# Performance work log

Hardware: AMD Instinct MI355X
Metric: run time of the kernel (lower is better)

The kernel has to match this reference:

```python
import jax, jax.numpy as jnp
import numpy as np

VOL = 128
FACTOR = 0.5 * VOL
N = 262144
LAT = 16
B = 8


def setup_inputs() -> dict:
    key = jax.random.key(0)
    ks = jax.random.split(key, 10)
    x = jax.random.normal(ks[0], (B, LAT), jnp.float32)
    inds = jax.random.randint(ks[1], (N, 3), 1, 126, dtype=jnp.int32)
    reference_values = jax.random.normal(ks[2], (N,), jnp.float32)
    # SIREN first layer: U(-1/in, 1/in)
    W0 = jax.random.uniform(ks[3], (LAT, 8), jnp.float32, -1.0 / LAT, 1.0 / LAT)
    b0 = jnp.zeros((8,), jnp.float32)
    # SIREN hidden layers (4 residual layers): U(-sqrt(6/in), sqrt(6/in))
    lim_h = float(np.sqrt(6.0 / 8.0))
    Wh = jax.random.uniform(ks[4], (4, 8, 8), jnp.float32, -lim_h, lim_h)
    bh = jnp.zeros((4, 8), jnp.float32)
    # final glorot-uniform layer: 8 -> 4N
    lim_f = float(np.sqrt(6.0 / (8.0 + 4.0 * N)))
    Wf = jax.random.uniform(ks[5], (8, 4 * N), jnp.float32, -lim_f, lim_f)
    bf = jnp.zeros((4 * N,), jnp.float32)
    return {"x": x, "W0": W0, "b0": b0, "Wh": Wh, "bh": bh, "Wf": Wf,
            "bf": bf, "reference_values": reference_values, "inds": inds}


def _siren_mlp(x, W0, b0, Wh, bh, Wf, bf):
    bf16 = jnp.bfloat16
    h = jnp.sin(30.0 * (x.astype(bf16) @ W0.astype(bf16) + b0.astype(bf16)))
    for i in range(Wh.shape[0]):  # 4 residual sine layers, 8-wide
        h = h + jnp.sin(h @ Wh[i].astype(bf16) + bh[i].astype(bf16))
    return h.astype(jnp.float32) @ Wf + bf  # [B, 4N], final layer in fp32


def reference(x, W0, b0, Wh, bh, Wf, bf, reference_values, inds):
    Bn = x.shape[0]
    out = _siren_mlp(x, W0, b0, Wh, bh, Wf, bf).reshape(Bn, N, 4)
    delta_coords, delta_values = out[..., :3], out[..., 3]
    # coords = stack(z,y,x reversed) normalized to [-1,1)
    coords_norm = (jnp.stack([inds[:, 2], inds[:, 1], inds[:, 0]], axis=1)
                   .astype(jnp.float32) - FACTOR) / FACTOR  # [N,3]
    values = reference_values + delta_values                 # [B,N]
    coords = FACTOR * (coords_norm[None] + delta_coords) + FACTOR  # [B,N,3]
    bposf = jnp.floor(coords)
    bposi = bposf.astype(jnp.int32)
    f = coords - bposf
    fx, fy, fz = f[..., 0], f[..., 1], f[..., 2]
    gx, gy, gz = 1.0 - fx, 1.0 - fy, 1.0 - fz
    # 8 trilinear weights, in the original concat order
    w = jnp.stack([gx * gy * gz, fx * gy * gz, gx * fy * gz, gx * gy * fz,
                   gx * fy * fz, fx * gy * fz, fx * fy * gz, fx * fy * fz],
                  axis=1)                                    # [B,8,N]
    bamp = (values[:, None, :] * w).reshape(Bn, 8 * N)
    offs = jnp.array([[0, 0, 0], [1, 0, 0], [0, 1, 0], [0, 0, 1],
                      [0, 1, 1], [1, 0, 1], [1, 1, 0], [1, 1, 1]], jnp.int32)
    bpos = (bposi[:, None, :, :] + offs[None, :, None, :]).reshape(Bn, 8 * N, 3)

    def scatter(pos, amp):
        return jnp.zeros((VOL, VOL, VOL), jnp.float32).at[
            pos[:, 2], pos[:, 1], pos[:, 0]].add(amp)

    grids = jax.vmap(scatter)(bpos, bamp)  # [B,128,128,128]
    return grids
```

## Files before the change

kernel.cpp:

```cpp
#include <hip/hip_runtime.h>
#include <math.h>

#define VOL   128
#define V2    (VOL*VOL)
#define V3    (VOL*VOL*VOL)
#define NPTS  262144
#define LATD  16
#define BATCH 8
#define FACTORF 64.0f
#define NBINS (VOL*VOL)
#define RZ 8
#define RY 4
#define REG_PER_B ((VOL/RZ)*(VOL/RY))
#define FAR_CAP 8192

#define WS_HBUF    0u
#define WS_HIST    256u
#define WS_START   65792u
#define WS_RANK    131344u
#define WS_KEYS    1179920u
#define WS_CTRL    1704208u
#define WS_FARLIST 1704240u
#define WS_COORDS  1737008u
#define WS_FULL    35291440u

__device__ __forceinline__ float bf16r(float x) {
    unsigned u = __float_as_uint(x);
    u = (u + 0x7fffu + ((u >> 16) & 1u)) & 0xffff0000u;
    return __uint_as_float(u);
}

__global__ void mlp_kernel(const float* __restrict__ x,
                           const float* __restrict__ W0,
                           const float* __restrict__ b0,
                           const float* __restrict__ Wh,
                           const float* __restrict__ bh,
                           float* __restrict__ hout) {
    int b = threadIdx.x;
    if (b >= BATCH) return;
    float xb[LATD];
    #pragma unroll
    for (int i = 0; i < LATD; ++i) xb[i] = bf16r(x[b*LATD + i]);
    float h[8];
    #pragma unroll
    for (int j = 0; j < 8; ++j) {
        float acc = 0.f;
        #pragma unroll
        for (int i = 0; i < LATD; ++i) acc += xb[i] * bf16r(W0[i*8 + j]);
        float t = bf16r(acc);
        t = bf16r(t + bf16r(b0[j]));
        t = bf16r(30.0f * t);
        h[j] = bf16r(sinf(t));
    }
    for (int l = 0; l < 4; ++l) {
        float nh[8];
        #pragma unroll
        for (int j = 0; j < 8; ++j) {
            float acc = 0.f;
            #pragma unroll
            for (int r = 0; r < 8; ++r) acc += h[r] * bf16r(Wh[(l*8 + r)*8 + j]);
            float t = bf16r(acc);
            t = bf16r(t + bf16r(bh[l*8 + j]));
            float s = bf16r(sinf(t));
            nh[j] = bf16r(h[j] + s);
        }
        #pragma unroll
        for (int j = 0; j < 8; ++j) h[j] = nh[j];
    }
    #pragma unroll
    for (int j = 0; j < 8; ++j) hout[b*8 + j] = h[j];
}

__global__ __launch_bounds__(256) void hist_rank_kernel(const int* __restrict__ inds,
                                                        unsigned* __restrict__ hist,
                                                        unsigned* __restrict__ rank) {
    int n = blockIdx.x * 256 + threadIdx.x;
    if (n >= NPTS) return;
    rank[n] = atomicAdd(&hist[inds[n*3]*VOL + inds[n*3+1]], 1u);
}

__global__ __launch_bounds__(256) void scan_kernel(const unsigned* __restrict__ hist,
                                                   unsigned* __restrict__ binstart,
                                                   unsigned* __restrict__ ctrl) {
    __shared__ unsigned part[256];
    int t = threadIdx.x;
    const int CH = NBINS / 256;
    unsigned s = 0;
    for (int k = 0; k < CH; ++k) s += hist[t*CH + k];
    part[t] = s; __syncthreads();
    for (int off = 1; off < 256; off <<= 1) {
        unsigned v = (t >= off) ? part[t - off] : 0u;
        __syncthreads();
        part[t] += v;
        __syncthreads();
    }
    unsigned run = (t == 0) ? 0u : part[t - 1];
    for (int k = 0; k < CH; ++k) {
        int idx = t*CH + k;
        binstart[idx] = run;
        run += hist[idx];
    }
    if (t == 0) { binstart[NBINS] = NPTS; ctrl[0] = 0u; ctrl[1] = 0u; }
}

__global__ __launch_bounds__(256) void coords_kernel(
    const float* __restrict__ Wf, const float* __restrict__ bfv_g,
    const float* __restrict__ rv, const int* __restrict__ inds,
    const float* __restrict__ hbuf, const unsigned* __restrict__ binstart,
    const unsigned* __restrict__ rank, unsigned short* __restrict__ keys,
    unsigned* __restrict__ ctrl, unsigned* __restrict__ farlist,
    float4* __restrict__ coords_s)
{
    __shared__ float hs[64];
    if (threadIdx.x < 64) hs[threadIdx.x] = hbuf[threadIdx.x];
    __syncthreads();
    int n = blockIdx.x * 256 + threadIdx.x;
    if (n >= NPTS) return;
    int iz = inds[n*3], iy = inds[n*3+1], ix = inds[n*3+2];
    float cnx = ((float)ix - FACTORF) / FACTORF;
    float cny = ((float)iy - FACTORF) / FACTORF;
    float cnz = ((float)iz - FACTORF) / FACTORF;
    float val0 = rv[n];
    float4 bfv = ((const float4*)bfv_g)[n];
    float4 wf[8];
    #pragma unroll
    for (int r = 0; r < 8; ++r)
        wf[r] = ((const float4*)(Wf + (size_t)r * 4 * NPTS))[n];
    unsigned pos = binstart[iz*VOL + iy] + rank[n];
    keys[pos] = (unsigned short)((iz << 7) | iy);
    #pragma unroll
    for (int b = 0; b < BATCH; ++b) {
        float o0 = bfv.x, o1 = bfv.y, o2 = bfv.z, o3 = bfv.w;
        #pragma unroll
        for (int r = 0; r < 8; ++r) {
            float hv = hs[b*8 + r];
            o0 = fmaf(hv, wf[r].x, o0);
            o1 = fmaf(hv, wf[r].y, o1);
            o2 = fmaf(hv, wf[r].z, o2);
            o3 = fmaf(hv, wf[r].w, o3);
        }
        float4 c;
        c.x = FACTORF * (cnx + o0) + FACTORF;
        c.y = FACTORF * (cny + o1) + FACTORF;
        c.z = FACTORF * (cnz + o2) + FACTORF;
        c.w = val0 + o3;
        coords_s[(size_t)b * NPTS + pos] = c;
        int bz = (int)floorf(c.z), by = (int)floorf(c.y);
        bool nearzy = ((unsigned)(bz - iz + 2) <= 4u) &&
                      ((unsigned)(by - iy + 2) <= 4u);
        if (!nearzy) {
            unsigned fp = atomicAdd(&ctrl[0], 1u);
            if (fp < FAR_CAP) farlist[fp] = (pos << 3) | (unsigned)b;
        }
    }
}

__global__ __launch_bounds__(256) void region_kernel(
    const float4* __restrict__ coords_s, const unsigned short* __restrict__ keys,
    const unsigned* __restrict__ binstart, float* __restrict__ out)
{
    __shared__ float tile[RZ*RY*VOL];
    __shared__ unsigned rstart[26], rcnt[26], rcum[27];
    int tid = threadIdx.x;
    int b   = blockIdx.x >> 9;
    int rid = blockIdx.x & (REG_PER_B - 1);
    int z0 = (rid >> 5) * RZ, y0 = (rid & 31) * RY;

    for (int i = tid; i < RZ*RY*VOL; i += 256) tile[i] = 0.f;

    if (tid < 13) {
        int zr = z0 - 3 + tid;
        int zz = (zr + VOL) & (VOL-1);
        int base = zz * VOL;
        int ylo = y0 - 3, yhi = y0 + RY + 2;
        int a0, a1, b0, b1;
        if (ylo < 0)        { a0 = ylo + VOL; a1 = VOL; b0 = 0; b1 = yhi; }
        else if (yhi > VOL) { a0 = ylo; a1 = VOL; b0 = 0; b1 = yhi - VOL; }
        else                { a0 = ylo; a1 = yhi; b0 = 0; b1 = 0; }
        unsigned sA = binstart[base + a0];
        rstart[tid*2]   = sA;
        rcnt[tid*2]     = binstart[base + a1] - sA;
        unsigned sB = binstart[base + b0];
        rstart[tid*2+1] = sB;
        rcnt[tid*2+1]   = (b1 > b0) ? (binstart[base + b1] - sB) : 0u;
    }
    __syncthreads();
    if (tid == 0) {
        unsigned run = 0;
        #pragma unroll
        for (int r = 0; r < 26; ++r) { rcum[r] = run; run += rcnt[r]; }
        rcum[26] = run;
    }
    __syncthreads();

    const int ox[8] = {0,1,0,0,0,1,1,1};
    const int oy[8] = {0,0,1,0,1,0,1,1};
    const int oz[8] = {0,0,0,1,1,1,0,1};
    const float4* cb = coords_s + (size_t)b * NPTS;

    unsigned total = rcum[26];
    int r = 0;
    for (unsigned f = tid; f < total; f += 1024) {
        float4 c[4]; unsigned kk[4]; bool v[4];
        #pragma unroll
        for (int u = 0; u < 4; ++u) {
            unsigned fu = f + (unsigned)u * 256u;
            v[u] = fu < total;
            if (v[u]) {
                while (fu >= rcum[r+1]) ++r;
                unsigned j = rstart[r] + (fu - rcum[r]);
                c[u]  = cb[j];
                kk[u] = keys[j];
            }
        }
        #pragma unroll
        for (int u = 0; u < 4; ++u) {
            if (!v[u]) continue;
            int piz = (int)(kk[u] >> 7), piy = (int)(kk[u] & 127u);
            float4 cc = c[u];
            float fxf = floorf(cc.x), fyf = floorf(cc.y), fzf = floorf(cc.z);
            int bx = (int)fxf, by = (int)fyf, bz = (int)fzf;
            bool nearzy = ((unsigned)(bz - piz + 2) <= 4u) &&
                          ((unsigned)(by - piy + 2) <= 4u);
            if (!nearzy) continue;
            float fx = cc.x - fxf, fy = cc.y - fyf, fz = cc.z - fzf;
            float gx = 1.f - fx, gy = 1.f - fy, gz = 1.f - fz;
            float val = cc.w;
            float w[8] = {gx*gy*gz, fx*gy*gz, gx*fy*gz, gx*gy*fz,
                          gx*fy*fz, fx*gy*fz, fx*fy*gz, fx*fy*fz};
            #pragma unroll
            for (int o = 0; o < 8; ++o) {
                int Z = (bz + oz[o]) & 127, dz = Z - z0;
                if ((unsigned)dz >= RZ) continue;
                int Y = (by + oy[o]) & 127, dy = Y - y0;
                if ((unsigned)dy >= RY) continue;
                int X = (bx + ox[o]) & 127;
                atomicAdd(&tile[(dz << 9) + (dy << 7) + X], val * w[o]);
            }
        }
    }
    __syncthreads();
    size_t ob = (size_t)b * V3;
    for (int i = tid; i < RZ*RY*VOL; i += 256) {
        int lz = i >> 9, ly = (i >> 7) & (RY-1), lx = i & 127;
        out[ob + (size_t)(z0+lz)*V2 + (y0+ly)*VOL + lx] = tile[i];
    }
}

__global__ __launch_bounds__(256) void far_kernel(
    const float4* __restrict__ coords_s, const unsigned* __restrict__ ctrl,
    const unsigned* __restrict__ farlist, float* __restrict__ out)
{
    unsigned cnt = ctrl[0];
    if (cnt > FAR_CAP) cnt = FAR_CAP;
    const int ox[8] = {0,1,0,0,0,1,1,1};
    const int oy[8] = {0,0,1,0,1,0,1,1};
    const int oz[8] = {0,0,0,1,1,1,0,1};
    for (unsigned idx = blockIdx.x * 256 + threadIdx.x; idx < cnt;
         idx += gridDim.x * 256) {
        unsigned e = farlist[idx];
        unsigned pos = e >> 3;
        int b = (int)(e & 7u);
        float4 c = coords_s[(size_t)b * NPTS + pos];
        float fxf = floorf(c.x), fyf = floorf(c.y), fzf = floorf(c.z);
        int bx = (int)fxf, by = (int)fyf, bz = (int)fzf;
        float fx = c.x - fxf, fy = c.y - fyf, fz = c.z - fzf;
        float gx = 1.f - fx, gy = 1.f - fy, gz = 1.f - fz;
        float val = c.w;
        float w[8] = {gx*gy*gz, fx*gy*gz, gx*fy*gz, gx*gy*fz,
                      gx*fy*fz, fx*gy*fz, fx*fy*gz, fx*fy*fz};
        float* ob = out + (size_t)b * V3;
        #pragma unroll
        for (int o = 0; o < 8; ++o) {
            int Z = (bz + oz[o]) & 127;
            int Y = (by + oy[o]) & 127;
            int X = (bx + ox[o]) & 127;
            atomicAdd(ob + (size_t)Z*V2 + Y*VOL + X, val * w[o]);
        }
    }
}

__global__ __launch_bounds__(256) void scatter_fallback(
    const float* __restrict__ Wf, const float* __restrict__ bfv_g,
    const float* __restrict__ rv, const int* __restrict__ inds,
    const float* __restrict__ hbuf, float* __restrict__ out)
{
    __shared__ float hs[BATCH*8];
    if (threadIdx.x < BATCH*8) hs[threadIdx.x] = hbuf[threadIdx.x];
    __syncthreads();
    int n = blockIdx.x * blockDim.x + threadIdx.x;
    if (n >= NPTS) return;
    int iz = inds[n*3 + 0], iy = inds[n*3 + 1], ix = inds[n*3 + 2];
    float cnx = ((float)ix - FACTORF) / FACTORF;
    float cny = ((float)iy - FACTORF) / FACTORF;
    float cnz = ((float)iz - FACTORF) / FACTORF;
    float val0 = rv[n];
    float4 bfv = ((const float4*)bfv_g)[n];
    float4 wf[8];
    #pragma unroll
    for (int r = 0; r < 8; ++r)
        wf[r] = ((const float4*)(Wf + (size_t)r * 4 * NPTS))[n];
    static const int offs[8][3] = {{0,0,0},{1,0,0},{0,1,0},{0,0,1},
                                   {0,1,1},{1,0,1},{1,1,0},{1,1,1}};
    #pragma unroll
    for (int b = 0; b < BATCH; ++b) {
        float o0 = bfv.x, o1 = bfv.y, o2 = bfv.z, o3 = bfv.w;
        #pragma unroll
        for (int r = 0; r < 8; ++r) {
            float hv = hs[b*8 + r];
            o0 = fmaf(hv, wf[r].x, o0);
            o1 = fmaf(hv, wf[r].y, o1);
            o2 = fmaf(hv, wf[r].z, o2);
            o3 = fmaf(hv, wf[r].w, o3);
        }
        float cx = FACTORF * (cnx + o0) + FACTORF;
        float cy = FACTORF * (cny + o1) + FACTORF;
        float cz = FACTORF * (cnz + o2) + FACTORF;
        float val = val0 + o3;
        float fxf = floorf(cx), fyf = floorf(cy), fzf = floorf(cz);
        int bx = (int)fxf, by = (int)fyf, bz = (int)fzf;
        float fx = cx - fxf, fy = cy - fyf, fz = cz - fzf;
        float gx = 1.f - fx, gy = 1.f - fy, gz = 1.f - fz;
        float w[8] = {gx*gy*gz, fx*gy*gz, gx*fy*gz, gx*gy*fz,
                      gx*fy*fz, fx*gy*fz, fx*fy*gz, fx*fy*fz};
        float* ob = out + (size_t)b * V3;
        #pragma unroll
        for (int o = 0; o < 8; ++o) {
            int X = (bx + offs[o][0]) & (VOL-1);
            int Y = (by + offs[o][1]) & (VOL-1);
            int Z = (bz + offs[o][2]) & (VOL-1);
            atomicAdd(ob + (size_t)Z*V2 + Y*VOL + X, val * w[o]);
        }
    }
}

extern "C" void kernel_launch(void* const* d_in, const int* in_sizes, int n_in,
                              void* d_out, int out_size, void* d_ws, size_t ws_size,
                              hipStream_t stream) {
    const float* x    = (const float*)d_in[0];
    const float* W0   = (const float*)d_in[1];
    const float* b0   = (const float*)d_in[2];
    const float* Wh   = (const float*)d_in[3];
    const float* bh   = (const float*)d_in[4];
    const float* Wf   = (const float*)d_in[5];
    const float* bf   = (const float*)d_in[6];
    const float* rv   = (const float*)d_in[7];
    const int*   inds = (const int*)d_in[8];
    float* out = (float*)d_out;
    char*  ws  = (char*)d_ws;

    float*          hbuf     = (float*)(ws + WS_HBUF);
    unsigned*       hist     = (unsigned*)(ws + WS_HIST);
    unsigned*       binstart = (unsigned*)(ws + WS_START);
    unsigned*       rank     = (unsigned*)(ws + WS_RANK);
    unsigned short* keys     = (unsigned short*)(ws + WS_KEYS);
    unsigned*       ctrl     = (unsigned*)(ws + WS_CTRL);
    unsigned*       farlist  = (unsigned*)(ws + WS_FARLIST);
    float4*         coords_s = (float4*)(ws + WS_COORDS);

    mlp_kernel<<<1, 64, 0, stream>>>(x, W0, b0, Wh, bh, hbuf);

    if (ws_size >= (size_t)WS_FULL) {
        hipMemsetAsync(hist, 0, NBINS*4, stream);
        hist_rank_kernel<<<NPTS/256, 256, 0, stream>>>(inds, hist, rank);
        scan_kernel<<<1, 256, 0, stream>>>(hist, binstart, ctrl);
        coords_kernel<<<NPTS/256, 256, 0, stream>>>(Wf, bf, rv, inds, hbuf,
                                                    binstart, rank, keys,
                                                    ctrl, farlist, coords_s);
        region_kernel<<<REG_PER_B*BATCH, 256, 0, stream>>>(coords_s, keys,
                                                           binstart, out);
        far_kernel<<<8, 256, 0, stream>>>(coords_s, ctrl, farlist, out);
    } else {
        hipMemsetAsync(d_out, 0, (size_t)out_size * sizeof(float), stream);
        scatter_fallback<<<NPTS/256, 256, 0, stream>>>(Wf, bf, rv, inds, hbuf, out);
    }
}
```

Before: 179.9 us.

## Parallelize bin scan, drop per-point keys array, reorder region blocks by batch

Replaces the single-block scan over 16K bins with a three-kernel multi-block scan. Removes the keys array: the region kernel now enumerates one range per (z,y) halo bin (13x9), so each point's source bin is known from shared memory instead of being loaded per point. Block index mapping interleaves batch fastest so neighbouring blocks share coords/binstart locality, and the inner loop is unrolled 8-wide for more loads in flight. It adds two extra launches and more ranges per block with a small shared-memory prefix scan.

```diff
diff --git a/kernel.cpp b/kernel.cpp
--- a/kernel.cpp
+++ b/kernel.cpp
@@ -12,15 +12,18 @@
 #define RZ 8
 #define RY 4
 #define REG_PER_B ((VOL/RZ)*(VOL/RY))
+#define HALO_Z 13
+#define HALO_Y 9
+#define NRANGE (HALO_Z*HALO_Y)
 #define FAR_CAP 8192
 
 #define WS_HBUF    0u
 #define WS_HIST    256u
 #define WS_START   65792u
 #define WS_RANK    131344u
-#define WS_KEYS    1179920u
-#define WS_CTRL    1704208u
-#define WS_FARLIST 1704240u
+#define WS_WGSUM   1179920u
+#define WS_CTRL    1180432u
+#define WS_FARLIST 1180464u
 #define WS_COORDS  1737008u
 #define WS_FULL    35291440u
 
@@ -79,35 +82,50 @@
     rank[n] = atomicAdd(&hist[inds[n*3]*VOL + inds[n*3+1]], 1u);
 }
 
-__global__ __launch_bounds__(256) void scan_kernel(const unsigned* __restrict__ hist,
+__global__ __launch_bounds__(256) void scanA_kernel(const unsigned* __restrict__ hist,
+                                                    unsigned* __restrict__ wgsum) {
+    __shared__ unsigned s[256];
+    int t = threadIdx.x;
+    s[t] = hist[blockIdx.x * 256 + t];
+    __syncthreads();
+    for (int off = 128; off > 0; off >>= 1) {
+        if (t < off) s[t] += s[t + off];
+        __syncthreads();
+    }
+    if (t == 0) wgsum[blockIdx.x] = s[0];
+}
+__global__ __launch_bounds__(64) void scanB_kernel(unsigned* __restrict__ wgsum,
                                                    unsigned* __restrict__ binstart,
                                                    unsigned* __restrict__ ctrl) {
-    __shared__ unsigned part[256];
+    if (threadIdx.x == 0) {
+        unsigned run = 0;
+        for (int i = 0; i < 64; ++i) { unsigned v = wgsum[i]; wgsum[i] = run; run += v; }
+        binstart[NBINS] = run;
+        ctrl[0] = 0u; ctrl[1] = 0u;
+    }
+}
+__global__ __launch_bounds__(256) void scanC_kernel(const unsigned* __restrict__ hist,
+                                                    const unsigned* __restrict__ wgsum,
+                                                    unsigned* __restrict__ binstart) {
+    __shared__ unsigned s[256];
     int t = threadIdx.x;
-    const int CH = NBINS / 256;
-    unsigned s = 0;
-    for (int k = 0; k < CH; ++k) s += hist[t*CH + k];
-    part[t] = s; __syncthreads();
+    int idx = blockIdx.x * 256 + t;
+    unsigned h = hist[idx];
+    s[t] = h; __syncthreads();
     for (int off = 1; off < 256; off <<= 1) {
-        unsigned v = (t >= off) ? part[t - off] : 0u;
-        __syncthreads();
-        part[t] += v;
-        __syncthreads();
-    }
-    unsigned run = (t == 0) ? 0u : part[t - 1];
-    for (int k = 0; k < CH; ++k) {
-        int idx = t*CH + k;
-        binstart[idx] = run;
-        run += hist[idx];
-    }
-    if (t == 0) { binstart[NBINS] = NPTS; ctrl[0] = 0u; ctrl[1] = 0u; }
+        unsigned v = (t >= off) ? s[t - off] : 0u;
+        __syncthreads();
+        s[t] += v;
+        __syncthreads();
+    }
+    binstart[idx] = s[t] - h + wgsum[blockIdx.x];
 }
 
 __global__ __launch_bounds__(256) void coords_kernel(
     const float* __restrict__ Wf, const float* __restrict__ bfv_g,
     const float* __restrict__ rv, const int* __restrict__ inds,
     const float* __restrict__ hbuf, const unsigned* __restrict__ binstart,
-    const unsigned* __restrict__ rank, unsigned short* __restrict__ keys,
+    const unsigned* __restrict__ rank,
     unsigned* __restrict__ ctrl, unsigned* __restrict__ farlist,
     float4* __restrict__ coords_s)
 {
@@ -127,7 +145,6 @@
     for (int r = 0; r < 8; ++r)
         wf[r] = ((const float4*)(Wf + (size_t)r * 4 * NPTS))[n];
     unsigned pos = binstart[iz*VOL + iy] + rank[n];
-    keys[pos] = (unsigned short)((iz << 7) | iy);
     #pragma unroll
     for (int b = 0; b < BATCH; ++b) {
         float o0 = bfv.x, o1 = bfv.y, o2 = bfv.z, o3 = bfv.w;
@@ -156,72 +173,68 @@
 }
 
 __global__ __launch_bounds__(256) void region_kernel(
-    const float4* __restrict__ coords_s, const unsigned short* __restrict__ keys,
+    const float4* __restrict__ coords_s,
     const unsigned* __restrict__ binstart, float* __restrict__ out)
 {
     __shared__ float tile[RZ*RY*VOL];
-    __shared__ unsigned rstart[26], rcnt[26], rcum[27];
+    __shared__ unsigned rstart[NRANGE];
+    __shared__ unsigned rcum[NRANGE+1];
+    __shared__ short rpz[NRANGE], rpy[NRANGE];
     int tid = threadIdx.x;
-    int b   = blockIdx.x >> 9;
-    int rid = blockIdx.x & (REG_PER_B - 1);
+    int b   = blockIdx.x & 7;
+    int rid = blockIdx.x >> 3;
     int z0 = (rid >> 5) * RZ, y0 = (rid & 31) * RY;
 
     for (int i = tid; i < RZ*RY*VOL; i += 256) tile[i] = 0.f;
 
-    if (tid < 13) {
-        int zr = z0 - 3 + tid;
-        int zz = (zr + VOL) & (VOL-1);
-        int base = zz * VOL;
-        int ylo = y0 - 3, yhi = y0 + RY + 2;
-        int a0, a1, b0, b1;
-        if (ylo < 0)        { a0 = ylo + VOL; a1 = VOL; b0 = 0; b1 = yhi; }
-        else if (yhi > VOL) { a0 = ylo; a1 = VOL; b0 = 0; b1 = yhi - VOL; }
-        else                { a0 = ylo; a1 = yhi; b0 = 0; b1 = 0; }
-        unsigned sA = binstart[base + a0];
-        rstart[tid*2]   = sA;
-        rcnt[tid*2]     = binstart[base + a1] - sA;
-        unsigned sB = binstart[base + b0];
-        rstart[tid*2+1] = sB;
-        rcnt[tid*2+1]   = (b1 > b0) ? (binstart[base + b1] - sB) : 0u;
-    }
-    __syncthreads();
-    if (tid == 0) {
-        unsigned run = 0;
-        #pragma unroll
-        for (int r = 0; r < 26; ++r) { rcum[r] = run; run += rcnt[r]; }
-        rcum[26] = run;
-    }
-    __syncthreads();
+    if (tid < NRANGE) {
+        int zi = tid / HALO_Y, yi = tid - zi * HALO_Y;
+        int zz = (z0 - 3 + zi) & (VOL-1);
+        int yy = (y0 - 3 + yi) & (VOL-1);
+        int base = zz * VOL + yy;
+        unsigned s = binstart[base];
+        rstart[tid] = s;
+        rpz[tid] = (short)zz; rpy[tid] = (short)yy;
+        rcum[tid+1] = binstart[base+1] - s;
+    }
+    if (tid == 0) rcum[0] = 0u;
+    __syncthreads();
+    for (int off = 1; off < NRANGE; off <<= 1) {
+        unsigned v = 0u;
+        if (tid < NRANGE && tid >= off) v = rcum[tid+1-off];
+        __syncthreads();
+        if (tid < NRANGE && tid >= off) rcum[tid+1] += v;
+        __syncthreads();
+    }
+    unsigned total = rcum[NRANGE];
 
     const int ox[8] = {0,1,0,0,0,1,1,1};
     const int oy[8] = {0,0,1,0,1,0,1,1};
     const int oz[8] = {0,0,0,1,1,1,0,1};
     const float4* cb = coords_s + (size_t)b * NPTS;
 
-    unsigned total = rcum[26];
     int r = 0;
-    for (unsigned f = tid; f < total; f += 1024) {
-        float4 c[4]; unsigned kk[4]; bool v[4];
-        #pragma unroll
-        for (int u = 0; u < 4; ++u) {
+    for (unsigned f = tid; f < total; f += 2048u) {
+        float4 c[8]; int pz[8], py[8]; bool v[8];
+        #pragma unroll
+        for (int u = 0; u < 8; ++u) {
             unsigned fu = f + (unsigned)u * 256u;
             v[u] = fu < total;
             if (v[u]) {
                 while (fu >= rcum[r+1]) ++r;
                 unsigned j = rstart[r] + (fu - rcum[r]);
-                c[u]  = cb[j];
-                kk[u] = keys[j];
+                c[u] = cb[j];
+                pz[u] = rpz[r]; py[u] = rpy[r];
             }
         }
         #pragma unroll
-        for (int u = 0; u < 4; ++u) {
+        for (int u = 0; u < 8; ++u) {
             if (!v[u]) continue;
-            int piz = (int)(kk[u] >> 7), piy = (int)(kk[u] & 127u);
             float4 cc = c[u];
             float fxf = floorf(cc.x), fyf = floorf(cc.y), fzf = floorf(cc.z);
             int bx = (int)fxf, by = (int)fyf, bz = (int)fzf;
-            bool nearzy = ((unsigned)(bz - piz + 2) <= 4u) &&
-                          ((unsigned)(by - piy + 2) <= 4u);
+            bool nearzy = ((unsigned)(bz - pz[u] + 2) <= 4u) &&
+                          ((unsigned)(by - py[u] + 2) <= 4u);
             if (!nearzy) continue;
             float fx = cc.x - fxf, fy = cc.y - fyf, fz = cc.z - fzf;
             float gx = 1.f - fx, gy = 1.f - fy, gz = 1.f - fz;
@@ -272,9 +285,9 @@
         float* ob = out + (size_t)b * V3;
         #pragma unroll
         for (int o = 0; o < 8; ++o) {
-            int Z = (bz + oz[o]) & 127;
-            int Y = (by + oy[o]) & 127;
-            int X = (bx + ox[o]) & 127;
+            int Z = (bz + oz[o]) & (VOL-1);
+            int Y = (by + oy[o]) & (VOL-1);
+            int X = (bx + ox[o]) & (VOL-1);
             atomicAdd(ob + (size_t)Z*V2 + Y*VOL + X, val * w[o]);
         }
     }
@@ -349,26 +362,27 @@
     float* out = (float*)d_out;
     char*  ws  = (char*)d_ws;
 
-    float*          hbuf     = (float*)(ws + WS_HBUF);
-    unsigned*       hist     = (unsigned*)(ws + WS_HIST);
-    unsigned*       binstart = (unsigned*)(ws + WS_START);
-    unsigned*       rank     = (unsigned*)(ws + WS_RANK);
-    unsigned short* keys     = (unsigned short*)(ws + WS_KEYS);
-    unsigned*       ctrl     = (unsigned*)(ws + WS_CTRL);
-    unsigned*       farlist  = (unsigned*)(ws + WS_FARLIST);
-    float4*         coords_s = (float4*)(ws + WS_COORDS);
+    float*    hbuf     = (float*)(ws + WS_HBUF);
+    unsigned* hist     = (unsigned*)(ws + WS_HIST);
+    unsigned* binstart = (unsigned*)(ws + WS_START);
+    unsigned* rank     = (unsigned*)(ws + WS_RANK);
+    unsigned* wgsum    = (unsigned*)(ws + WS_WGSUM);
+    unsigned* ctrl     = (unsigned*)(ws + WS_CTRL);
+    unsigned* farlist  = (unsigned*)(ws + WS_FARLIST);
+    float4*   coords_s = (float4*)(ws + WS_COORDS);
 
     mlp_kernel<<<1, 64, 0, stream>>>(x, W0, b0, Wh, bh, hbuf);
 
     if (ws_size >= (size_t)WS_FULL) {
         hipMemsetAsync(hist, 0, NBINS*4, stream);
         hist_rank_kernel<<<NPTS/256, 256, 0, stream>>>(inds, hist, rank);
-        scan_kernel<<<1, 256, 0, stream>>>(hist, binstart, ctrl);
+        scanA_kernel<<<64, 256, 0, stream>>>(hist, wgsum);
+        scanB_kernel<<<1, 64, 0, stream>>>(wgsum, binstart, ctrl);
+        scanC_kernel<<<64, 256, 0, stream>>>(hist, wgsum, binstart);
         coords_kernel<<<NPTS/256, 256, 0, stream>>>(Wf, bf, rv, inds, hbuf,
-                                                    binstart, rank, keys,
+                                                    binstart, rank,
                                                     ctrl, farlist, coords_s);
-        region_kernel<<<REG_PER_B*BATCH, 256, 0, stream>>>(coords_s, keys,
-                                                           binstart, out);
+        region_kernel<<<REG_PER_B*BATCH, 256, 0, stream>>>(coords_s, binstart, out);
         far_kernel<<<8, 256, 0, stream>>>(coords_s, ctrl, farlist, out);
     } else {
         hipMemsetAsync(d_out, 0, (size_t)out_size * sizeof(float), stream);
```

New measurement: 188.3 us. 1.05x slower.

## Parallelize bin prefix scan across 64 workgroups and batch region gather loads

Applied to the files above, without the earlier changes.

Replaces the single-workgroup 16K-bin exclusive scan with a three-phase scan: per-workgroup reduction, a tiny serial scan of 64 partial sums, then a per-workgroup local scan plus offset. This targets the serial latency of one block walking 64 bins per thread. The region kernel also computes all four gather indices first and then issues the coordinate and key loads together, to raise memory-level parallelism. The change adds two kernel launches and a small workspace slot carved from the far-list capacity.

```diff
diff --git a/kernel.cpp b/kernel.cpp
--- a/kernel.cpp
+++ b/kernel.cpp
@@ -12,7 +12,7 @@
 #define RZ 8
 #define RY 4
 #define REG_PER_B ((VOL/RZ)*(VOL/RY))
-#define FAR_CAP 8192
+#define FAR_CAP 8128
 
 #define WS_HBUF    0u
 #define WS_HIST    256u
@@ -20,7 +20,8 @@
 #define WS_RANK    131344u
 #define WS_KEYS    1179920u
 #define WS_CTRL    1704208u
-#define WS_FARLIST 1704240u
+#define WS_WGSUM   1704240u
+#define WS_FARLIST 1704496u
 #define WS_COORDS  1737008u
 #define WS_FULL    35291440u
 
@@ -79,28 +80,43 @@
     rank[n] = atomicAdd(&hist[inds[n*3]*VOL + inds[n*3+1]], 1u);
 }
 
-__global__ __launch_bounds__(256) void scan_kernel(const unsigned* __restrict__ hist,
+__global__ __launch_bounds__(256) void scanA_kernel(const unsigned* __restrict__ hist,
+                                                    unsigned* __restrict__ wgsum) {
+    __shared__ unsigned s[256];
+    int t = threadIdx.x;
+    s[t] = hist[blockIdx.x * 256 + t];
+    __syncthreads();
+    for (int off = 128; off > 0; off >>= 1) {
+        if (t < off) s[t] += s[t + off];
+        __syncthreads();
+    }
+    if (t == 0) wgsum[blockIdx.x] = s[0];
+}
+__global__ __launch_bounds__(64) void scanB_kernel(unsigned* __restrict__ wgsum,
                                                    unsigned* __restrict__ binstart,
                                                    unsigned* __restrict__ ctrl) {
-    __shared__ unsigned part[256];
+    if (threadIdx.x == 0) {
+        unsigned run = 0;
+        for (int i = 0; i < 64; ++i) { unsigned v = wgsum[i]; wgsum[i] = run; run += v; }
+        binstart[NBINS] = run;
+        ctrl[0] = 0u; ctrl[1] = 0u;
+    }
+}
+__global__ __launch_bounds__(256) void scanC_kernel(const unsigned* __restrict__ hist,
+                                                    const unsigned* __restrict__ wgsum,
+                                                    unsigned* __restrict__ binstart) {
+    __shared__ unsigned s[256];
     int t = threadIdx.x;
-    const int CH = NBINS / 256;
-    unsigned s = 0;
-    for (int k = 0; k < CH; ++k) s += hist[t*CH + k];
-    part[t] = s; __syncthreads();
+    int idx = blockIdx.x * 256 + t;
+    unsigned h = hist[idx];
+    s[t] = h; __syncthreads();
     for (int off = 1; off < 256; off <<= 1) {
-        unsigned v = (t >= off) ? part[t - off] : 0u;
+        unsigned v = (t >= off) ? s[t - off] : 0u;
         __syncthreads();
-        part[t] += v;
+        s[t] += v;
         __syncthreads();
     }
-    unsigned run = (t == 0) ? 0u : part[t - 1];
-    for (int k = 0; k < CH; ++k) {
-        int idx = t*CH + k;
-        binstart[idx] = run;
-        run += hist[idx];
-    }
-    if (t == 0) { binstart[NBINS] = NPTS; ctrl[0] = 0u; ctrl[1] = 0u; }
+    binstart[idx] = s[t] - h + wgsum[blockIdx.x];
 }
 
 __global__ __launch_bounds__(256) void coords_kernel(
@@ -201,16 +217,22 @@
     unsigned total = rcum[26];
     int r = 0;
     for (unsigned f = tid; f < total; f += 1024) {
-        float4 c[4]; unsigned kk[4]; bool v[4];
+        unsigned j[4]; bool v[4];
         #pragma unroll
         for (int u = 0; u < 4; ++u) {
             unsigned fu = f + (unsigned)u * 256u;
             v[u] = fu < total;
             if (v[u]) {
                 while (fu >= rcum[r+1]) ++r;
-                unsigned j = rstart[r] + (fu - rcum[r]);
-                c[u]  = cb[j];
-                kk[u] = keys[j];
+                j[u] = rstart[r] + (fu - rcum[r]);
+            }
+        }
+        float4 c[4]; unsigned kk[4];
+        #pragma unroll
+        for (int u = 0; u < 4; ++u) {
+            if (v[u]) {
+                c[u]  = cb[j[u]];
+                kk[u] = keys[j[u]];
             }
         }
         #pragma unroll
@@ -272,9 +294,9 @@
         float* ob = out + (size_t)b * V3;
         #pragma unroll
         for (int o = 0; o < 8; ++o) {
-            int Z = (bz + oz[o]) & 127;
-            int Y = (by + oy[o]) & 127;
-            int X = (bx + ox[o]) & 127;
+            int Z = (bz + oz[o]) & (VOL-1);
+            int Y = (by + oy[o]) & (VOL-1);
+            int X = (bx + ox[o]) & (VOL-1);
             atomicAdd(ob + (size_t)Z*V2 + Y*VOL + X, val * w[o]);
         }
     }
@@ -355,6 +377,7 @@
     unsigned*       rank     = (unsigned*)(ws + WS_RANK);
     unsigned short* keys     = (unsigned short*)(ws + WS_KEYS);
     unsigned*       ctrl     = (unsigned*)(ws + WS_CTRL);
+    unsigned*       wgsum    = (unsigned*)(ws + WS_WGSUM);
     unsigned*       farlist  = (unsigned*)(ws + WS_FARLIST);
     float4*         coords_s = (float4*)(ws + WS_COORDS);
 
@@ -363,7 +386,9 @@
     if (ws_size >= (size_t)WS_FULL) {
         hipMemsetAsync(hist, 0, NBINS*4, stream);
         hist_rank_kernel<<<NPTS/256, 256, 0, stream>>>(inds, hist, rank);
-        scan_kernel<<<1, 256, 0, stream>>>(hist, binstart, ctrl);
+        scanA_kernel<<<64, 256, 0, stream>>>(hist, wgsum);
+        scanB_kernel<<<1, 64, 0, stream>>>(wgsum, binstart, ctrl);
+        scanC_kernel<<<64, 256, 0, stream>>>(hist, wgsum, binstart);
         coords_kernel<<<NPTS/256, 256, 0, stream>>>(Wf, bf, rv, inds, hbuf,
                                                     binstart, rank, keys,
                                                     ctrl, farlist, coords_s);
```

New measurement: 179.5 us. About the same (-0.3%).
